# Performance work log

Hardware: AMD Instinct MI355X
Metric: run time of the kernel (lower is better)

The kernel has to match this reference:

```python
import jax, jax.numpy as jnp
import numpy as np

T, B, E = 48, 16, 512
V, S, G = 50000, 40000, 32
K_VAL, NUM_C = 8, 20


def setup_inputs() -> dict:
    key = jax.random.key(0)
    ks = jax.random.split(key, 5)
    return {
        "word_embeddings": jax.random.normal(ks[0], (T, B, E), jnp.float32),
        "prev_word_embeddings": jax.random.normal(ks[1], (T, B, E), jnp.float32),
        "location_context": jnp.zeros((T, B, E), jnp.float32),
        "logits_globals": jax.random.normal(ks[2], (T * B, V), jnp.float32),
        "SC": jax.random.normal(ks[3], (S, E), jnp.float32),
        "neighbours_table": jax.random.randint(ks[4], (V, G), 0, S, jnp.int32),
        "K": K_VAL,
        "num_C": NUM_C,
    }


def reference(word_embeddings, prev_word_embeddings, location_context,
              logits_globals, SC, neighbours_table, K, num_C):
    T_, B_, E_ = word_embeddings.shape
    S_ = SC.shape[0]
    G_ = neighbours_table.shape[1]

    # --- update_context_average: sliding-window (box-filter) sum via cumsum ---
    cat = jnp.concatenate([prev_word_embeddings, word_embeddings], axis=0)  # [2T,B,E]
    cs = jnp.cumsum(cat, axis=0)
    win = cs[T_:2 * T_] - cs[T_ - num_C:2 * T_ - num_C]
    loc_ctx = location_context + win / num_C                                 # [T,B,E]

    # --- top-K globals -> padded sense-neighbour gather ---
    _, topk = jax.lax.top_k(logits_globals, K)                               # [T*B,K]
    neigh = neighbours_table[topk]                                           # [T*B,K,G]
    all_sense_neighbours = neigh.reshape(T_, B_, K * G_)                     # [T,B,KG]
    senses_context = SC[all_sense_neighbours]                                # [T,B,KG,E]

    # --- cosine similarity (torch.nn.CosineSimilarity, eps=1e-8) ---
    eps = 1e-8
    a = loc_ctx[:, :, None, :]                                               # [T,B,1,E]
    an = jnp.maximum(jnp.linalg.norm(a, axis=-1), eps)
    bn = jnp.maximum(jnp.linalg.norm(senses_context, axis=-1), eps)
    cos = jnp.sum(a * senses_context, axis=-1) / (an * bn)                   # [T,B,KG]

    # --- pick best sense, scatter into epsilon-softmax ---
    first_idx = jnp.argmax(cos, axis=2)                                      # [T,B]
    first_sense = jnp.take_along_axis(
        all_sense_neighbours, first_idx[:, :, None], axis=2)[:, :, 0]        # [T,B]
    chosen = 1.0 - eps * (S_ - 1)
    sm = jnp.full((T_, B_, S_), eps, jnp.float32)
    tt = jnp.arange(T_)[:, None]
    bb = jnp.arange(B_)[None, :]
    sm = sm.at[tt, bb, first_sense].set(chosen)
    predictions_senses = jnp.log(sm).reshape(T_ * B_, S_)

    predictions_globals = jax.nn.log_softmax(logits_globals, axis=1)
    return predictions_globals, predictions_senses
```

## Files before the change

kernel.cpp:

```cpp
#include <hip/hip_runtime.h>
#include <cstdint>
#include <cmath>

#define T_ 48
#define B_ 16
#define E_ 512
#define V_ 50000
#define S_ 40000
#define G_ 32
#define K_ 8
#define NUMC 20
#define ROWS (T_*B_)
#define V4 (V_/4)
#define E4 (E_/4)
#define NCAND 1024

__global__ __launch_bounds__(256) void k_locctx(const float4* __restrict__ word,
                                                const float4* __restrict__ prev,
                                                const float4* __restrict__ locc,
                                                float4* __restrict__ out) {
    int f = blockIdx.x * 256 + threadIdx.x;
    if (f >= T_ * B_ * E4) return;
    int e4 = f % E4;
    int tb = f / E4;
    int b = tb % B_;
    int t = tb / B_;
    float4 acc = make_float4(0.f, 0.f, 0.f, 0.f);
    #pragma unroll
    for (int d = 0; d < NUMC; ++d) {
        int src = t - d;
        float4 v;
        if (src >= 0) v = word[(src * B_ + b) * E4 + e4];
        else          v = prev[((T_ + src) * B_ + b) * E4 + e4];
        acc.x += v.x; acc.y += v.y; acc.z += v.z; acc.w += v.w;
    }
    float4 l = locc[f];
    out[f] = make_float4(l.x + acc.x / (float)NUMC,
                         l.y + acc.y / (float)NUMC,
                         l.z + acc.z / (float)NUMC,
                         l.w + acc.w / (float)NUMC);
}

__global__ __launch_bounds__(512) void k_topk_lse(const float* __restrict__ logits,
                                                  int* __restrict__ topk,
                                                  float* __restrict__ lse) {
    __shared__ float smax[512];
    __shared__ float cand_v[NCAND];
    __shared__ int   cand_i[NCAND];
    __shared__ int   ncand;
    __shared__ float s_m, s_tau;
    __shared__ float ssum[8];

    int row = blockIdx.x;
    int tid = threadIdx.x;
    int lane = tid & 63, w = tid >> 6;
    const float4* rp = (const float4*)(logits + (size_t)row * V_);

    float m = -INFINITY;
    for (int it = tid; it < V4; it += 512) {
        float4 v = rp[it];
        m = fmaxf(m, fmaxf(fmaxf(v.x, v.y), fmaxf(v.z, v.w)));
    }
    smax[tid] = m;
    if (tid == 0) ncand = 0;
    __syncthreads();

    if (tid < 64) {
        float v8[8];
        #pragma unroll
        for (int j = 0; j < 8; ++j) v8[j] = smax[tid * 8 + j];
        #pragma unroll
        for (int r = 0; r < 8; ++r) {
            float lm = v8[0];
            #pragma unroll
            for (int j = 1; j < 8; ++j) lm = fmaxf(lm, v8[j]);
            #pragma unroll
            for (int mask = 1; mask < 64; mask <<= 1)
                lm = fmaxf(lm, __shfl_xor(lm, mask));
            if (tid == 0) {
                if (r == 0) s_m = lm;
                if (r == 7) s_tau = lm;
            }
            #pragma unroll
            for (int j = 0; j < 8; ++j) if (v8[j] == lm) v8[j] = -INFINITY;
        }
    }
    __syncthreads();

    float rm  = s_m;
    float tau = s_tau;
    const float L2E = 1.4426950408889634f;
    float nml2 = -rm * L2E;

    float sum = 0.f;
    for (int it = tid; it < V4; it += 512) {
        float4 v = rp[it];
        float xs[4] = {v.x, v.y, v.z, v.w};
        #pragma unroll
        for (int c = 0; c < 4; ++c) {
            float x = xs[c];
            sum += __builtin_exp2f(__builtin_fmaf(x, L2E, nml2));
            if (x >= tau) {
                int p = atomicAdd(&ncand, 1);
                if (p < NCAND) { cand_v[p] = x; cand_i[p] = it * 4 + c; }
            }
        }
    }
    #pragma unroll
    for (int off = 32; off; off >>= 1) sum += __shfl_down(sum, off);
    if (lane == 0) ssum[w] = sum;
    __syncthreads();

    if (tid == 0) {
        float tot = ssum[0];
        #pragma unroll
        for (int i = 1; i < 8; ++i) tot += ssum[i];
        lse[row] = rm + logf(tot);
    }

    if (tid < 64) {
        int C = ncand; if (C > NCAND) C = NCAND;
        for (int r = 0; r < 8; ++r) {
            float bv = -INFINITY; int bi = 0x7fffffff;
            for (int c = tid; c < C; c += 64) {
                float v = cand_v[c]; int i = cand_i[c];
                if (v > bv || (v == bv && i < bi)) { bv = v; bi = i; }
            }
            #pragma unroll
            for (int mask = 1; mask < 64; mask <<= 1) {
                float ov = __shfl_xor(bv, mask);
                int   oi = __shfl_xor(bi, mask);
                if (ov > bv || (ov == bv && oi < bi)) { bv = ov; bi = oi; }
            }
            if (tid == 0) topk[row * K_ + r] = bi;
            for (int c = tid; c < C; c += 64)
                if (cand_i[c] == bi) { cand_v[c] = -INFINITY; cand_i[c] = 0x7fffffff; }
        }
    }
}

__global__ __launch_bounds__(256) void k_logsoftmax(const float4* __restrict__ logits,
                                                    const float* __restrict__ lse,
                                                    float4* __restrict__ out) {
    int row = blockIdx.y;
    int i4 = blockIdx.x * 256 + threadIdx.x;
    if (i4 >= V4) return;
    float l = lse[row];
    size_t o = (size_t)row * V4 + i4;
    float4 v = logits[o];
    out[o] = make_float4(v.x - l, v.y - l, v.z - l, v.w - l);
}

__global__ __launch_bounds__(256) void k_fill(float4* __restrict__ out, float val, int n4) {
    int i = blockIdx.x * 256 + threadIdx.x;
    if (i < n4) out[i] = make_float4(val, val, val, val);
}

__global__ __launch_bounds__(512) void k_sense(const float* __restrict__ loc,
                                               const int* __restrict__ topk,
                                               const int* __restrict__ neigh,
                                               const float* __restrict__ SC,
                                               float* __restrict__ outS,
                                               float log_chosen) {
    __shared__ __align__(16) float a[E_];
    __shared__ int   sidx[K_ * G_];
    __shared__ float warr[8];
    __shared__ float wbv[8];
    __shared__ int   wbn[8];
    __shared__ float a_n;

    int row = blockIdx.x;
    int tid = threadIdx.x;
    int lane = tid & 63, w = tid >> 6;

    float a0 = loc[(size_t)row * E_ + tid];
    a[tid] = a0;
    if (tid < K_ * G_)
        sidx[tid] = neigh[(size_t)topk[row * K_ + (tid >> 5)] * G_ + (tid & 31)];

    float p = a0 * a0;
    #pragma unroll
    for (int off = 32; off; off >>= 1) p += __shfl_down(p, off);
    if (lane == 0) warr[w] = p;
    __syncthreads();
    if (tid == 0) {
        float t = warr[0];
        #pragma unroll
        for (int i = 1; i < 8; ++i) t += warr[i];
        a_n = fmaxf(sqrtf(t), 1e-8f);
    }
    __syncthreads();

    const float4* a4 = (const float4*)a;
    float4 aA = a4[lane], aB = a4[lane + 64];
    float an = a_n;

    float best = -INFINITY; int bn = 0x7fffffff;
    for (int n = w; n < K_ * G_; n += 16) {
        int n2 = n + 8;
        const float4* sp0 = (const float4*)(SC + (size_t)sidx[n]  * E_);
        const float4* sp1 = (const float4*)(SC + (size_t)sidx[n2] * E_);
        float4 s0A = sp0[lane], s0B = sp0[lane + 64];
        float4 s1A = sp1[lane], s1B = sp1[lane + 64];
        float dot0 = s0A.x * aA.x + s0A.y * aA.y + s0A.z * aA.z + s0A.w * aA.w
                   + s0B.x * aB.x + s0B.y * aB.y + s0B.z * aB.z + s0B.w * aB.w;
        float nr0  = s0A.x * s0A.x + s0A.y * s0A.y + s0A.z * s0A.z + s0A.w * s0A.w
                   + s0B.x * s0B.x + s0B.y * s0B.y + s0B.z * s0B.z + s0B.w * s0B.w;
        float dot1 = s1A.x * aA.x + s1A.y * aA.y + s1A.z * aA.z + s1A.w * aA.w
                   + s1B.x * aB.x + s1B.y * aB.y + s1B.z * aB.z + s1B.w * aB.w;
        float nr1  = s1A.x * s1A.x + s1A.y * s1A.y + s1A.z * s1A.z + s1A.w * s1A.w
                   + s1B.x * s1B.x + s1B.y * s1B.y + s1B.z * s1B.z + s1B.w * s1B.w;
        #pragma unroll
        for (int off = 32; off; off >>= 1) {
            dot0 += __shfl_down(dot0, off);
            nr0  += __shfl_down(nr0,  off);
            dot1 += __shfl_down(dot1, off);
            nr1  += __shfl_down(nr1,  off);
        }
        if (lane == 0) {
            float cs0 = dot0 / (an * fmaxf(sqrtf(nr0), 1e-8f));
            if (cs0 > best) { best = cs0; bn = n; }
            float cs1 = dot1 / (an * fmaxf(sqrtf(nr1), 1e-8f));
            if (cs1 > best) { best = cs1; bn = n2; }
        }
    }
    if (lane == 0) { wbv[w] = best; wbn[w] = bn; }
    __syncthreads();
    if (tid == 0) {
        float bv = wbv[0]; int bnn = wbn[0];
        #pragma unroll
        for (int i = 1; i < 8; ++i) {
            if (wbv[i] > bv || (wbv[i] == bv && wbn[i] < bnn)) { bv = wbv[i]; bnn = wbn[i]; }
        }
        outS[(size_t)row * S_ + sidx[bnn]] = log_chosen;
    }
}

extern "C" void kernel_launch(void* const* d_in, const int* in_sizes, int n_in,
                              void* d_out, int out_size, void* d_ws, size_t ws_size,
                              hipStream_t stream) {
    const float* word   = (const float*)d_in[0];
    const float* prev   = (const float*)d_in[1];
    const float* locc   = (const float*)d_in[2];
    const float* logits = (const float*)d_in[3];
    const float* SC     = (const float*)d_in[4];
    const int*   neigh  = (const int*)d_in[5];

    float* out_g = (float*)d_out;
    float* out_s = out_g + (size_t)ROWS * V_;

    float* loc  = (float*)d_ws;
    int*   topk = (int*)(loc + (size_t)T_ * B_ * E_);
    float* lse  = (float*)(topk + ROWS * K_);

    k_locctx<<<dim3((T_ * B_ * E4 + 255) / 256), 256, 0, stream>>>(
        (const float4*)word, (const float4*)prev, (const float4*)locc, (float4*)loc);

    k_topk_lse<<<ROWS, 512, 0, stream>>>(logits, topk, lse);

    k_logsoftmax<<<dim3((V4 + 255) / 256, ROWS), 256, 0, stream>>>(
        (const float4*)logits, lse, (float4*)out_g);

    float fillv = logf(1e-8f);
    k_fill<<<(ROWS * (S_ / 4) + 255) / 256, 256, 0, stream>>>(
        (float4*)out_s, fillv, ROWS * (S_ / 4));

    float log_chosen = logf(1.0f - 1e-8f * (float)(S_ - 1));
    k_sense<<<ROWS, 512, 0, stream>>>(loc, topk, neigh, SC, out_s, log_chosen);
}
```

Measured before the change: 546.1 us.

## Fuse top-k, online logsumexp and log-softmax; fold fill and context into sense kernel

Replaces the separate max pass with a single pass over each logits row. That pass computes an online logsumexp and keeps a per-thread sorted top-8 list, and candidates are then filtered by the threshold. The log-softmax output is written from the same kernel with nontemporal stores, which removes a separate launch and its full re-read of logits. The epsilon fill of the senses output and the sliding-window context average move into the sense kernel, cutting five launches to two and dropping the workspace round trips. The per-element top-8 insertion adds branchy work in the streaming loop, and the fused log-softmax re-reads the row, which may or may not still be in cache.

Measured after the change: 628.4 us. +15.1%, slower.

```diff
diff --git a/kernel.cpp b/kernel.cpp
--- a/kernel.cpp
+++ b/kernel.cpp
@@ -13,110 +13,105 @@
 #define ROWS (T_*B_)
 #define V4 (V_/4)
 #define E4 (E_/4)
-#define NCAND 1024
-
-__global__ __launch_bounds__(256) void k_locctx(const float4* __restrict__ word,
-                                                const float4* __restrict__ prev,
-                                                const float4* __restrict__ locc,
-                                                float4* __restrict__ out) {
-    int f = blockIdx.x * 256 + threadIdx.x;
-    if (f >= T_ * B_ * E4) return;
-    int e4 = f % E4;
-    int tb = f / E4;
-    int b = tb % B_;
-    int t = tb / B_;
-    float4 acc = make_float4(0.f, 0.f, 0.f, 0.f);
-    #pragma unroll
-    for (int d = 0; d < NUMC; ++d) {
-        int src = t - d;
-        float4 v;
-        if (src >= 0) v = word[(src * B_ + b) * E4 + e4];
-        else          v = prev[((T_ + src) * B_ + b) * E4 + e4];
-        acc.x += v.x; acc.y += v.y; acc.z += v.z; acc.w += v.w;
-    }
-    float4 l = locc[f];
-    out[f] = make_float4(l.x + acc.x / (float)NUMC,
-                         l.y + acc.y / (float)NUMC,
-                         l.z + acc.z / (float)NUMC,
-                         l.w + acc.w / (float)NUMC);
-}
-
-__global__ __launch_bounds__(512) void k_topk_lse(const float* __restrict__ logits,
-                                                  int* __restrict__ topk,
-                                                  float* __restrict__ lse) {
+#define NCAND 4096
+
+typedef float floatx4 __attribute__((ext_vector_type(4)));
+
+__global__ __launch_bounds__(512) void k_topk_lse_lsm(const float* __restrict__ logits,
+                                                      int* __restrict__ topk,
+                                                      float* __restrict__ out_g) {
     __shared__ float smax[512];
+    __shared__ float wm[8], ws[8];
     __shared__ float cand_v[NCAND];
     __shared__ int   cand_i[NCAND];
     __shared__ int   ncand;
-    __shared__ float s_m, s_tau;
-    __shared__ float ssum[8];
+    __shared__ float s_tau, s_lse;
 
     int row = blockIdx.x;
     int tid = threadIdx.x;
     int lane = tid & 63, w = tid >> 6;
     const float4* rp = (const float4*)(logits + (size_t)row * V_);
-
-    float m = -INFINITY;
-    for (int it = tid; it < V4; it += 512) {
-        float4 v = rp[it];
-        m = fmaxf(m, fmaxf(fmaxf(v.x, v.y), fmaxf(v.z, v.w)));
-    }
-    smax[tid] = m;
-    if (tid == 0) ncand = 0;
-    __syncthreads();
-
-    if (tid < 64) {
-        float v8[8];
-        #pragma unroll
-        for (int j = 0; j < 8; ++j) v8[j] = smax[tid * 8 + j];
-        #pragma unroll
-        for (int r = 0; r < 8; ++r) {
-            float lm = v8[0];
-            #pragma unroll
-            for (int j = 1; j < 8; ++j) lm = fmaxf(lm, v8[j]);
-            #pragma unroll
-            for (int mask = 1; mask < 64; mask <<= 1)
-                lm = fmaxf(lm, __shfl_xor(lm, mask));
-            if (tid == 0) {
-                if (r == 0) s_m = lm;
-                if (r == 7) s_tau = lm;
-            }
-            #pragma unroll
-            for (int j = 0; j < 8; ++j) if (v8[j] == lm) v8[j] = -INFINITY;
-        }
-    }
-    __syncthreads();
-
-    float rm  = s_m;
-    float tau = s_tau;
     const float L2E = 1.4426950408889634f;
-    float nml2 = -rm * L2E;
-
-    float sum = 0.f;
+
+    float v8[8]; int i8[8];
+    #pragma unroll
+    for (int j = 0; j < 8; ++j) { v8[j] = -INFINITY; i8[j] = 0x7fffffff; }
+    float m = -INFINITY, s = 0.f;
+
     for (int it = tid; it < V4; it += 512) {
         float4 v = rp[it];
         float xs[4] = {v.x, v.y, v.z, v.w};
         #pragma unroll
         for (int c = 0; c < 4; ++c) {
             float x = xs[c];
-            sum += __builtin_exp2f(__builtin_fmaf(x, L2E, nml2));
-            if (x >= tau) {
-                int p = atomicAdd(&ncand, 1);
-                if (p < NCAND) { cand_v[p] = x; cand_i[p] = it * 4 + c; }
+            if (x > v8[7]) {
+                v8[7] = x; i8[7] = it * 4 + c;
+                #pragma unroll
+                for (int k = 7; k >= 1; --k) {
+                    bool sw = v8[k] > v8[k-1];
+                    float tv = sw ? v8[k-1] : v8[k];
+                    int   ti = sw ? i8[k-1] : i8[k];
+                    v8[k-1] = sw ? v8[k] : v8[k-1];
+                    i8[k-1] = sw ? i8[k] : i8[k-1];
+                    v8[k] = tv; i8[k] = ti;
+                }
             }
-        }
-    }
-    #pragma unroll
-    for (int off = 32; off; off >>= 1) sum += __shfl_down(sum, off);
-    if (lane == 0) ssum[w] = sum;
-    __syncthreads();
-
-    if (tid == 0) {
-        float tot = ssum[0];
-        #pragma unroll
-        for (int i = 1; i < 8; ++i) tot += ssum[i];
-        lse[row] = rm + logf(tot);
-    }
+            if (x > m) { s *= __builtin_exp2f((m - x) * L2E); m = x; }
+            s += __builtin_exp2f((x - m) * L2E);
+        }
+    }
+    smax[tid] = m;
+
+    float mm = m, sacc = s;
+    #pragma unroll
+    for (int off = 32; off; off >>= 1) {
+        float om = __shfl_down(mm, off);
+        float os = __shfl_down(sacc, off);
+        float M = fmaxf(mm, om);
+        sacc = sacc * __builtin_exp2f((mm - M) * L2E) + os * __builtin_exp2f((om - M) * L2E);
+        mm = M;
+    }
+    if (lane == 0) { wm[w] = mm; ws[w] = sacc; }
+    if (tid == 0) ncand = 0;
+    __syncthreads();
+
+    if (tid < 64) {
+        float t8[8];
+        #pragma unroll
+        for (int j = 0; j < 8; ++j) t8[j] = smax[tid * 8 + j];
+        #pragma unroll
+        for (int r = 0; r < 8; ++r) {
+            float lm = t8[0];
+            #pragma unroll
+            for (int j = 1; j < 8; ++j) lm = fmaxf(lm, t8[j]);
+            #pragma unroll
+            for (int mask = 1; mask < 64; mask <<= 1)
+                lm = fmaxf(lm, __shfl_xor(lm, mask));
+            if (tid == 0 && r == 7) s_tau = lm;
+            #pragma unroll
+            for (int j = 0; j < 8; ++j) if (t8[j] == lm) t8[j] = -INFINITY;
+        }
+        if (tid == 0) {
+            float M = wm[0];
+            #pragma unroll
+            for (int i = 1; i < 8; ++i) M = fmaxf(M, wm[i]);
+            float S = 0.f;
+            #pragma unroll
+            for (int i = 0; i < 8; ++i) S += ws[i] * __builtin_exp2f((wm[i] - M) * L2E);
+            s_lse = M + logf(S);
+        }
+    }
+    __syncthreads();
+
+    float tau = s_tau;
+    #pragma unroll
+    for (int j = 0; j < 8; ++j) {
+        if (v8[j] >= tau) {
+            int p = atomicAdd(&ncand, 1);
+            if (p < NCAND) { cand_v[p] = v8[j]; cand_i[p] = i8[j]; }
+        }
+    }
+    __syncthreads();
 
     if (tid < 64) {
         int C = ncand; if (C > NCAND) C = NCAND;
@@ -137,31 +132,24 @@
                 if (cand_i[c] == bi) { cand_v[c] = -INFINITY; cand_i[c] = 0x7fffffff; }
         }
     }
+
+    float l = s_lse;
+    floatx4* og = (floatx4*)(out_g + (size_t)row * V_);
+    for (int it = tid; it < V4; it += 512) {
+        float4 v = rp[it];
+        floatx4 o = {v.x - l, v.y - l, v.z - l, v.w - l};
+        __builtin_nontemporal_store(o, og + it);
+    }
 }
 
-__global__ __launch_bounds__(256) void k_logsoftmax(const float4* __restrict__ logits,
-                                                    const float* __restrict__ lse,
-                                                    float4* __restrict__ out) {
-    int row = blockIdx.y;
-    int i4 = blockIdx.x * 256 + threadIdx.x;
-    if (i4 >= V4) return;
-    float l = lse[row];
-    size_t o = (size_t)row * V4 + i4;
-    float4 v = logits[o];
-    out[o] = make_float4(v.x - l, v.y - l, v.z - l, v.w - l);
-}
-
-__global__ __launch_bounds__(256) void k_fill(float4* __restrict__ out, float val, int n4) {
-    int i = blockIdx.x * 256 + threadIdx.x;
-    if (i < n4) out[i] = make_float4(val, val, val, val);
-}
-
-__global__ __launch_bounds__(512) void k_sense(const float* __restrict__ loc,
+__global__ __launch_bounds__(512) void k_sense(const float* __restrict__ word,
+                                               const float* __restrict__ prev,
+                                               const float* __restrict__ locc,
                                                const int* __restrict__ topk,
                                                const int* __restrict__ neigh,
                                                const float* __restrict__ SC,
                                                float* __restrict__ outS,
-                                               float log_chosen) {
+                                               float log_eps, float log_chosen) {
     __shared__ __align__(16) float a[E_];
     __shared__ int   sidx[K_ * G_];
     __shared__ float warr[8];
@@ -170,24 +158,38 @@
     __shared__ float a_n;
 
     int row = blockIdx.x;
+    int t = row / B_, b = row % B_;
     int tid = threadIdx.x;
     int lane = tid & 63, w = tid >> 6;
 
-    float a0 = loc[(size_t)row * E_ + tid];
+    float acc = 0.f;
+    #pragma unroll
+    for (int d = 0; d < NUMC; ++d) {
+        int src = t - d;
+        const float* p = (src >= 0) ? (word + (size_t)(src * B_ + b) * E_)
+                                    : (prev + (size_t)((T_ + src) * B_ + b) * E_);
+        acc += p[tid];
+    }
+    float a0 = locc[(size_t)row * E_ + tid] + acc / (float)NUMC;
     a[tid] = a0;
     if (tid < K_ * G_)
         sidx[tid] = neigh[(size_t)topk[row * K_ + (tid >> 5)] * G_ + (tid & 31)];
 
-    float p = a0 * a0;
-    #pragma unroll
-    for (int off = 32; off; off >>= 1) p += __shfl_down(p, off);
-    if (lane == 0) warr[w] = p;
+    floatx4 fv = {log_eps, log_eps, log_eps, log_eps};
+    floatx4* orow = (floatx4*)(outS + (size_t)row * S_);
+    for (int i = tid; i < S_ / 4; i += 512)
+        __builtin_nontemporal_store(fv, orow + i);
+
+    float pp = a0 * a0;
+    #pragma unroll
+    for (int off = 32; off; off >>= 1) pp += __shfl_down(pp, off);
+    if (lane == 0) warr[w] = pp;
     __syncthreads();
     if (tid == 0) {
-        float t = warr[0];
-        #pragma unroll
-        for (int i = 1; i < 8; ++i) t += warr[i];
-        a_n = fmaxf(sqrtf(t), 1e-8f);
+        float tt = warr[0];
+        #pragma unroll
+        for (int i = 1; i < 8; ++i) tt += warr[i];
+        a_n = fmaxf(sqrtf(tt), 1e-8f);
     }
     __syncthreads();
 
@@ -249,22 +251,12 @@
     float* out_g = (float*)d_out;
     float* out_s = out_g + (size_t)ROWS * V_;
 
-    float* loc  = (float*)d_ws;
-    int*   topk = (int*)(loc + (size_t)T_ * B_ * E_);
-    float* lse  = (float*)(topk + ROWS * K_);
-
-    k_locctx<<<dim3((T_ * B_ * E4 + 255) / 256), 256, 0, stream>>>(
-        (const float4*)word, (const float4*)prev, (const float4*)locc, (float4*)loc);
-
-    k_topk_lse<<<ROWS, 512, 0, stream>>>(logits, topk, lse);
-
-    k_logsoftmax<<<dim3((V4 + 255) / 256, ROWS), 256, 0, stream>>>(
-        (const float4*)logits, lse, (float4*)out_g);
-
-    float fillv = logf(1e-8f);
-    k_fill<<<(ROWS * (S_ / 4) + 255) / 256, 256, 0, stream>>>(
-        (float4*)out_s, fillv, ROWS * (S_ / 4));
-
+    int* topk = (int*)d_ws;
+
+    k_topk_lse_lsm<<<ROWS, 512, 0, stream>>>(logits, topk, out_g);
+
+    float log_eps    = logf(1e-8f);
     float log_chosen = logf(1.0f - 1e-8f * (float)(S_ - 1));
-    k_sense<<<ROWS, 512, 0, stream>>>(loc, topk, neigh, SC, out_s, log_chosen);
+    k_sense<<<ROWS, 512, 0, stream>>>(word, prev, locc, topk, neigh, SC,
+                                      out_s, log_eps, log_chosen);
 }
```
